# Performance work log

Hardware: AMD Instinct MI355X
Metric: run time of the kernel (lower is better)

The kernel has to match this reference:

```python
import jax, jax.numpy as jnp
import numpy as np


def setup_inputs() -> dict:
    key = jax.random.key(0)
    ks = jax.random.split(key, 6)
    B, T, DIM = 8, 2048, 512
    CB_DIM, CB_SIZE = 256, 8192
    return {
        "x": jax.random.normal(ks[0], (B, T, DIM), dtype=jnp.float32),
        "embed": jax.random.normal(ks[1], (CB_SIZE, CB_DIM), dtype=jnp.float32),
        "W_in": jax.random.normal(ks[2], (CB_DIM, DIM), dtype=jnp.float32) * (1.0 / np.sqrt(DIM)),
        "b_in": jax.random.normal(ks[3], (CB_DIM,), dtype=jnp.float32) * 0.01,
        "W_out": jax.random.normal(ks[4], (DIM, CB_DIM), dtype=jnp.float32) * (1.0 / np.sqrt(CB_DIM)),
        "b_out": jax.random.normal(ks[5], (DIM,), dtype=jnp.float32) * 0.01,
    }


def reference(x, embed, W_in, b_in, W_out, b_out):
    """encode (project_in -> euclidean quantize) then decode (embedding -> project_out).

    Returns (embed_ind [B,T] int32, out [B,T,dim] float).
    """
    B, T, _ = x.shape
    # project_in: Linear(dim -> codebook_dim)
    z = jnp.einsum("btd,cd->btc", x, W_in) + b_in            # [B,T,CB_DIM]
    zf = z.reshape(-1, z.shape[-1])                           # [N,CB_DIM]
    # dist = -(||z||^2 - 2 z.e + ||e||^2); argmax over codebook
    x_sq = jnp.sum(zf * zf, axis=1, keepdims=True)            # [N,1]
    e_sq = jnp.sum(embed * embed, axis=1)                     # [CB_SIZE]
    dist = -(x_sq - 2.0 * (zf @ embed.T) + e_sq[None, :])     # [N,CB_SIZE]
    embed_ind = jnp.argmax(dist, axis=-1).reshape(B, T)       # [B,T]
    # decode: embedding lookup + project_out
    quantize = embed[embed_ind]                               # [B,T,CB_DIM]
    out = jnp.einsum("btc,dc->btd", quantize, W_out) + b_out  # [B,T,dim]
    return embed_ind, out
```

## Files before the change

### kernel.cpp

```cpp
#include <hip/hip_runtime.h>

#define N_TOK 16384
#define DIM   512
#define CBD   256
#define CBS   8192

typedef short short8 __attribute__((ext_vector_type(8)));
typedef float f32x4 __attribute__((ext_vector_type(4)));

#define GLOAD16(g, l) __builtin_amdgcn_global_load_lds( \
    (const __attribute__((address_space(1))) void*)(g), \
    (__attribute__((address_space(3))) void*)(l), 16, 0, 0)

#define VMCNT(n) asm volatile("s_waitcnt vmcnt(" #n ")" ::: "memory")

__device__ inline unsigned short f2bf_rne(float f) {
    unsigned u = __float_as_uint(f);
    unsigned r = (u + 0x7FFFu + ((u >> 16) & 1u)) >> 16;
    return (unsigned short)r;
}
__device__ inline float bf2f(unsigned short h) { return __uint_as_float((unsigned)h << 16); }
__device__ inline short f2h(float f) {
    _Float16 h = (_Float16)f;
    short r; __builtin_memcpy(&r, &h, 2); return r;
}
__device__ inline float h2f(short s) {
    _Float16 h; __builtin_memcpy(&h, &s, 2); return (float)h;
}

template <int LOGK>
__global__ __launch_bounds__(256) void pack_w(const float* __restrict__ src, short* __restrict__ dst) {
    int e = blockIdx.x * 256 + threadIdx.x;
    int r = e >> LOGK, k = e & ((1 << LOGK) - 1);
    float v = src[e];
    unsigned short h = f2bf_rne(v);
    unsigned short l = f2bf_rne(v - bf2f(h));
    size_t base = (size_t)r << (LOGK + 1);
    dst[base + k] = (short)h;
    dst[base + (1 << LOGK) + k] = (short)l;
}

__global__ __launch_bounds__(256) void prep_embed(const float* __restrict__ embed,
                                                  float* __restrict__ esq,
                                                  short* __restrict__ epack,
                                                  short* __restrict__ e16,
                                                  float* __restrict__ denorm) {
    int wave = threadIdx.x >> 6, lane = threadIdx.x & 63;
    int c = (blockIdx.x << 2) + wave;
    float4 v = reinterpret_cast<const float4*>(embed + (size_t)c * CBD)[lane];
    short4 hs, ls, fs;
    {
        unsigned short h, l;
        h = f2bf_rne(v.x); l = f2bf_rne(v.x - bf2f(h)); hs.x = h; ls.x = l;
        h = f2bf_rne(v.y); l = f2bf_rne(v.y - bf2f(h)); hs.y = h; ls.y = l;
        h = f2bf_rne(v.z); l = f2bf_rne(v.z - bf2f(h)); hs.z = h; ls.z = l;
        h = f2bf_rne(v.w); l = f2bf_rne(v.w - bf2f(h)); hs.w = h; ls.w = l;
    }
    fs.x = f2h(v.x); fs.y = f2h(v.y); fs.z = f2h(v.z); fs.w = f2h(v.w);
    reinterpret_cast<short4*>(epack + (size_t)c * 512)[lane] = hs;
    reinterpret_cast<short4*>(epack + (size_t)c * 512 + 256)[lane] = ls;
    reinterpret_cast<short4*>(e16 + (size_t)c * 256)[lane] = fs;
    float s = v.x * v.x + v.y * v.y + v.z * v.z + v.w * v.w;
    float dx = v.x - h2f(fs.x), dy = v.y - h2f(fs.y);
    float dz = v.z - h2f(fs.z), dw = v.w - h2f(fs.w);
    float ds = dx * dx + dy * dy + dz * dz + dw * dw;
    #pragma unroll
    for (int m = 32; m; m >>= 1) { s += __shfl_xor(s, m, 64); ds += __shfl_xor(ds, m, 64); }
    if (!lane) { esq[c] = s; denorm[c] = ds; }
}

__global__ __launch_bounds__(256) void znorm_k(const float* __restrict__ zf32,
                                               const short* __restrict__ z16,
                                               float2* __restrict__ znorm2) {
    int wave = threadIdx.x >> 6, lane = threadIdx.x & 63;
    int r = blockIdx.x * 4 + wave;
    float4 v = reinterpret_cast<const float4*>(zf32 + (size_t)r * 256)[lane];
    short4 h = reinterpret_cast<const short4*>(z16 + (size_t)r * 256)[lane];
    float a = h2f(h.x), b = h2f(h.y), c = h2f(h.z), d = h2f(h.w);
    float s16 = a * a + b * b + c * c + d * d;
    float dx = v.x - a, dy = v.y - b, dz = v.z - c, dw = v.w - d;
    float ds = dx * dx + dy * dy + dz * dz + dw * dw;
    #pragma unroll
    for (int m = 32; m; m >>= 1) { s16 += __shfl_xor(s16, m, 64); ds += __shfl_xor(ds, m, 64); }
    if (!lane) znorm2[r] = make_float2(sqrtf(s16), sqrtf(ds));
}

__global__ __launch_bounds__(256) void maxe_k(const float* __restrict__ esq,
                                              const float* __restrict__ denorm,
                                              float* __restrict__ maxe) {
    float m = 0.f, md = 0.f;
    #pragma unroll
    for (int k = 0; k < 32; ++k) {
        m = fmaxf(m, esq[threadIdx.x + (k << 8)]);
        md = fmaxf(md, denorm[threadIdx.x + (k << 8)]);
    }
    #pragma unroll
    for (int s = 32; s; s >>= 1) {
        m = fmaxf(m, __shfl_xor(m, s, 64));
        md = fmaxf(md, __shfl_xor(md, s, 64));
    }
    __shared__ float w[4], wd[4];
    if (!(threadIdx.x & 63)) { w[threadIdx.x >> 6] = m; wd[threadIdx.x >> 6] = md; }
    __syncthreads();
    if (threadIdx.x == 0) {
        maxe[0] = sqrtf(fmaxf(fmaxf(w[0], w[1]), fmaxf(w[2], w[3])));
        maxe[1] = sqrtf(fmaxf(fmaxf(wd[0], wd[1]), fmaxf(wd[2], wd[3])));
    }
}

__global__ __launch_bounds__(256, 3) void gemm_in_mfma(const short* __restrict__ xpk,
                                                       const short* __restrict__ wpk,
                                                       const float* __restrict__ b_in,
                                                       short* __restrict__ z16,
                                                       float* __restrict__ zf32) {
    __shared__ __align__(16) char smem[49152];
    const int tid = threadIdx.x;
    const int lane = tid & 63, wid = tid >> 6;
    const int l15 = lane & 15, rg = lane >> 4;
    const int bm = blockIdx.x << 6, bn = blockIdx.y << 7;
    const int g = tid & 7, rpb = tid >> 3;

    const char* xb = (const char*)xpk;
    const char* wb = (const char*)wpk;
    const int sw = ((g ^ (rpb & 7)) << 4);
    size_t aoff[2], boff[2][2];
    #pragma unroll
    for (int it = 0; it < 2; ++it)
        aoff[it] = (size_t)(bm + it * 32 + rpb) * 2048 + sw;
    #pragma unroll
    for (int it = 0; it < 4; ++it)
        boff[it >> 1][it & 1] = (size_t)(bn + it * 32 + rpb) * 2048 + sw;

    const int ax0 = ((rg ^ (l15 & 7)) << 4);
    const int ax1 = (((rg + 4) ^ (l15 & 7)) << 4);
    const char* aBase = smem + l15 * 128;
    const char* bBase = smem + 8192 + (wid * 32 + l15) * 128;

    f32x4 acc[4][2] = {};

#define GIN_STAGE(BUF, KT) do { \
    size_t aK = (size_t)(((((KT) >> 4) << 3) | ((KT) & 7))) * 128; \
    size_t bK = (size_t)((((((KT) >> 3) & 1) << 3) | ((KT) & 7))) * 128; \
    char* dA = smem + (BUF) * 24576 + (tid << 4); \
    char* dB = dA + 8192; \
    GLOAD16(xb + aoff[0] + aK, dA); \
    GLOAD16(xb + aoff[1] + aK, dA + 4096); \
    GLOAD16(wb + boff[0][0] + bK, dB); \
    GLOAD16(wb + boff[0][1] + bK, dB + 4096); \
    GLOAD16(wb + boff[1][0] + bK, dB + 8192); \
    GLOAD16(wb + boff[1][1] + bK, dB + 12288); } while (0)

    GIN_STAGE(0, 0);
    VMCNT(0);
    __syncthreads();
    #pragma unroll 1
    for (int kt = 0; kt < 32; ++kt) {
        const int buf = kt & 1;
        if (kt + 1 < 32) GIN_STAGE(buf ^ 1, kt + 1);
        const char* aB = aBase + buf * 24576;
        const char* bB = bBase + buf * 24576;
        #pragma unroll
        for (int ks = 0; ks < 2; ++ks) {
            int ax = ks ? ax1 : ax0;
            short8 aF[4], bF[2];
            #pragma unroll
            for (int mi = 0; mi < 4; ++mi) aF[mi] = *(const short8*)(aB + mi * 2048 + ax);
            #pragma unroll
            for (int ni = 0; ni < 2; ++ni) bF[ni] = *(const short8*)(bB + ni * 2048 + ax);
            #pragma unroll
            for (int mi = 0; mi < 4; ++mi)
                #pragma unroll
                for (int ni = 0; ni < 2; ++ni)
                    acc[mi][ni] = __builtin_amdgcn_mfma_f32_16x16x32_bf16(aF[mi], bF[ni], acc[mi][ni], 0, 0, 0);
        }
        VMCNT(0);
        __syncthreads();
    }
    float bb[2];
    #pragma unroll
    for (int ni = 0; ni < 2; ++ni) bb[ni] = b_in[bn + wid * 32 + ni * 16 + l15];
    #pragma unroll
    for (int mi = 0; mi < 4; ++mi)
        #pragma unroll
        for (int ni = 0; ni < 2; ++ni)
            #pragma unroll
            for (int j = 0; j < 4; ++j) {
                int r = bm + mi * 16 + rg * 4 + j;
                int c = bn + wid * 32 + ni * 16 + l15;
                float s = acc[mi][ni][j] + bb[ni];
                z16[(size_t)r * 256 + c] = f2h(s);
                zf32[(size_t)r * 256 + c] = s;
            }
}

__global__ __launch_bounds__(512, 2) void score_mfma(const short* __restrict__ zpk,
                                                     const short* __restrict__ epk,
                                                     const float* __restrict__ esqg,
                                                     float4* __restrict__ partials) {
    __shared__ __align__(16) char smem[131072];
    const int tid = threadIdx.x;
    const int lane = tid & 63, w = tid >> 6;
    const int l15 = lane & 15, rg = lane >> 4;

    int flat = blockIdx.x;
    int xcd = flat & 7, jb = flat >> 3;
    int g  = xcd >> 1;
    int bX = ((xcd & 1) << 5) + jb;
    const int bm = bX << 8;
    const int C0g = g << 11;

    const char* zb = (const char*)zpk;
    short8 aF0[8], aF1[8];
    #pragma unroll
    for (int ks = 0; ks < 8; ++ks) {
        aF0[ks] = *(const short8*)(zb + (size_t)(bm + w * 32 + l15) * 512 + ks * 64 + rg * 16);
        aF1[ks] = *(const short8*)(zb + (size_t)(bm + w * 32 + 16 + l15) * 512 + ks * 64 + rg * 16);
    }

    const char* eb = (const char*)epk;

#define SCB_STAGE(BUF, T) do { \
    _Pragma("unroll") for (int i_ = 0; i_ < 8; ++i_) { \
        int u_ = i_ * 512 + tid; \
        int col_ = u_ >> 5, slot_ = u_ & 31; \
        const char* s_ = eb + (size_t)(C0g + (T) * 128 + col_) * 512 \
                         + ((slot_ ^ (col_ & 15)) << 4); \
        GLOAD16(s_, smem + (BUF) * 65536 + u_ * 16); \
    } } while (0)

    f32x4 acc0[8] = {};
    f32x4 acc1[8] = {};

    SCB_STAGE(0, 0);
    VMCNT(0);
    __syncthreads();

    #pragma unroll 1
    for (int ch = 0; ch < 16; ++ch) {
        const int buf = ch & 1;
        if (ch < 15) SCB_STAGE(buf ^ 1, ch + 1);
        const char* bB = smem + buf * 65536;
        #pragma unroll
        for (int ks = 0; ks < 8; ++ks) {
            short8 bF[8];
            #pragma unroll
            for (int ni = 0; ni < 8; ++ni)
                bF[ni] = *(const short8*)(bB + (ni * 16 + l15) * 512 +
                                          (((ks * 4 + rg) ^ (l15 & 15)) << 4));
            #pragma unroll
            for (int ni = 0; ni < 8; ++ni) {
                acc0[ni] = __builtin_amdgcn_mfma_f32_16x16x32_f16(aF0[ks], bF[ni], acc0[ni], 0, 0, 0);
                acc1[ni] = __builtin_amdgcn_mfma_f32_16x16x32_f16(aF1[ks], bF[ni], acc1[ni], 0, 0, 0);
            }
        }
        {
            const int cb = C0g + ch * 128 + l15;
            float esq8[8];
            #pragma unroll
            for (int ni = 0; ni < 8; ++ni) esq8[ni] = esqg[cb + ni * 16];
            #pragma unroll
            for (int mi = 0; mi < 2; ++mi)
                #pragma unroll
                for (int j2 = 0; j2 < 4; ++j2) {
                    float v1 = -3.4e38f, v2 = -3.4e38f;
                    int i1 = 0x7fffffff;
                    #pragma unroll
                    for (int ni = 0; ni < 8; ++ni) {
                        float s = fmaf(2.f, mi ? acc1[ni][j2] : acc0[ni][j2], -esq8[ni]);
                        int c = cb + ni * 16;
                        if (s > v1) { v2 = v1; v1 = s; i1 = c; }
                        else if (s > v2) v2 = s;
                    }
                    #pragma unroll
                    for (int m = 1; m < 16; m <<= 1) {
                        float ov1 = __shfl_xor(v1, m, 64);
                        int   oi1 = __shfl_xor(i1, m, 64);
                        float ov2 = __shfl_xor(v2, m, 64);
                        float nv2 = fmaxf(fmaxf(v2, ov2), fminf(v1, ov1));
                        if (ov1 > v1 || (ov1 == v1 && oi1 < i1)) { v1 = ov1; i1 = oi1; }
                        v2 = nv2;
                    }
                    if (l15 == 0) {
                        int row = bm + w * 32 + mi * 16 + rg * 4 + j2;
                        partials[(size_t)(g * 16 + ch) * N_TOK + row] =
                            make_float4(v1, __int_as_float(i1), v2, 0.f);
                    }
                }
            #pragma unroll
            for (int ni = 0; ni < 8; ++ni) {
                acc0[ni] = (f32x4){0.f, 0.f, 0.f, 0.f};
                acc1[ni] = (f32x4){0.f, 0.f, 0.f, 0.f};
            }
        }
        VMCNT(0);
        __syncthreads();
    }
}

__global__ __launch_bounds__(256) void combine(const float4* __restrict__ partials,
                                               const float2* __restrict__ znorm2,
                                               const float* __restrict__ maxe,
                                               int* __restrict__ idx, float* __restrict__ idxf,
                                               float* __restrict__ rescueT) {
    int sub = threadIdx.x & 63;
    int row = blockIdx.x * 4 + (threadIdx.x >> 6);
    float4 p = partials[(size_t)sub * N_TOK + row];
    float v1 = p.x; int i1 = __float_as_int(p.y); float v2 = p.z;
    #pragma unroll
    for (int m = 1; m < 64; m <<= 1) {
        float ov1 = __shfl_xor(v1, m, 64);
        int   oi1 = __shfl_xor(i1, m, 64);
        float ov2 = __shfl_xor(v2, m, 64);
        float nv2 = fmaxf(fmaxf(v2, ov2), fminf(v1, ov1));
        if (ov1 > v1 || (ov1 == v1 && oi1 < i1)) { v1 = ov1; i1 = oi1; }
        v2 = nv2;
    }
    if (sub == 0) {
        float2 zn = znorm2[row];
        float thr = fmaf(2.1f, zn.y * maxe[0] + zn.x * maxe[1], 0.02f);
        idx[row] = i1;
        idxf[row] = (float)i1;
        rescueT[row] = (v1 - v2 <= thr) ? (v1 - thr) : 3.0e38f;
    }
}

__global__ __launch_bounds__(256) void rescue(const float* __restrict__ zf32,
                                              const float* __restrict__ embed,
                                              const float* __restrict__ esq,
                                              const float4* __restrict__ partials,
                                              const float* __restrict__ rescueT,
                                              int* __restrict__ idx, float* __restrict__ idxf) {
    int row = blockIdx.x;
    float t = rescueT[row];
    if (t > 1.0e38f) return;
    __shared__ __align__(16) float zrow[256];
    __shared__ float gv[16];
    __shared__ int   gi[16];
    const int tid = threadIdx.x;
    const int grp = tid >> 4, ln = tid & 15;
    zrow[tid] = zf32[(size_t)row * 256 + tid];
    __syncthreads();
    const float4* zr = (const float4*)zrow;
    float bv = -3.4e38f; int bi = 0x7fffffff;
    for (int nt = 0; nt < 64; ++nt) {
        if (partials[(size_t)nt * N_TOK + row].x < t) continue;
        #pragma unroll 1
        for (int it = 0; it < 8; ++it) {
            int c = nt * 128 + it * 16 + grp;
            const float4* er = (const float4*)(embed + (size_t)c * 256);
            float d = 0.f;
            #pragma unroll
            for (int q = 0; q < 4; ++q) {
                float4 e4 = er[q * 16 + ln];
                float4 z4 = zr[q * 16 + ln];
                d = fmaf(e4.x, z4.x, d); d = fmaf(e4.y, z4.y, d);
                d = fmaf(e4.z, z4.z, d); d = fmaf(e4.w, z4.w, d);
            }
            #pragma unroll
            for (int m = 1; m < 16; m <<= 1) d += __shfl_xor(d, m, 64);
            if (ln == 0) {
                float s = 2.f * d - esq[c];
                if (s > bv || (s == bv && c < bi)) { bv = s; bi = c; }
            }
        }
    }
    if (ln == 0) { gv[grp] = bv; gi[grp] = bi; }
    __syncthreads();
    if (tid == 0) {
        float v = gv[0]; int i = gi[0];
        #pragma unroll
        for (int k = 1; k < 16; ++k)
            if (gv[k] > v || (gv[k] == v && gi[k] < i)) { v = gv[k]; i = gi[k]; }
        idx[row] = i; idxf[row] = (float)i;
    }
}

__global__ __launch_bounds__(256, 2) void gemm_out_mfma(const short* __restrict__ epk,
                                                        const short* __restrict__ wpk,
                                                        const int* __restrict__ idx,
                                                        const float* __restrict__ b_out,
                                                        float* __restrict__ out) {
    __shared__ __align__(16) char smem[65536];
    const int tid = threadIdx.x;
    const int lane = tid & 63, wid = tid >> 6;
    const int wr = wid >> 1, wc = wid & 1;
    const int l15 = lane & 15, rg = lane >> 4;
    const int bm = blockIdx.x << 7, bn = blockIdx.y << 7;
    const int g = tid & 7, rpb = tid >> 3;

    const char* ebp = (const char*)epk;
    const char* wb = (const char*)wpk;
    const int sw = ((g ^ (rpb & 7)) << 4);
    size_t aoff[4], boff[4];
    #pragma unroll
    for (int it = 0; it < 4; ++it) {
        int c = idx[bm + it * 32 + rpb];
        aoff[it] = (size_t)c * 1024 + sw;
        boff[it] = (size_t)(bn + it * 32 + rpb) * 1024 + sw;
    }

    const int ax0 = ((rg ^ (l15 & 7)) << 4);
    const int ax1 = (((rg + 4) ^ (l15 & 7)) << 4);
    const char* aBase = smem + (wr * 64 + l15) * 128;
    const char* bBase = smem + 16384 + (wc * 64 + l15) * 128;

    f32x4 acc[4][4] = {};

#define GOUT_STAGE(BUF, KT) do { \
    size_t aK = (size_t)((((KT) & 3) | (((KT) >> 3) << 2))) * 128; \
    size_t bK = (size_t)((KT) & 7) * 128; \
    char* dA = smem + (BUF) * 32768 + (tid << 4); \
    char* dB = dA + 16384; \
    _Pragma("unroll") for (int it_ = 0; it_ < 4; ++it_) { \
        GLOAD16(ebp + aoff[it_] + aK, dA + it_ * 4096); \
        GLOAD16(wb + boff[it_] + bK, dB + it_ * 4096); } } while (0)

    GOUT_STAGE(0, 0);
    VMCNT(0);
    __syncthreads();
    #pragma unroll 1
    for (int kt = 0; kt < 16; ++kt) {
        const int buf = kt & 1;
        if (kt + 1 < 16) GOUT_STAGE(buf ^ 1, kt + 1);
        const char* aB = aBase + buf * 32768;
        const char* bB = bBase + buf * 32768;
        #pragma unroll
        for (int ks = 0; ks < 2; ++ks) {
            int ax = ks ? ax1 : ax0;
            short8 aF[4], bF[4];
            #pragma unroll
            for (int mi = 0; mi < 4; ++mi) aF[mi] = *(const short8*)(aB + mi * 2048 + ax);
            #pragma unroll
            for (int ni = 0; ni < 4; ++ni) bF[ni] = *(const short8*)(bB + ni * 2048 + ax);
            #pragma unroll
            for (int mi = 0; mi < 4; ++mi)
                #pragma unroll
                for (int ni = 0; ni < 4; ++ni)
                    acc[mi][ni] = __builtin_amdgcn_mfma_f32_16x16x32_bf16(aF[mi], bF[ni], acc[mi][ni], 0, 0, 0);
        }
        VMCNT(0);
        __syncthreads();
    }
    float bb[4];
    #pragma unroll
    for (int ni = 0; ni < 4; ++ni) bb[ni] = b_out[bn + wc * 64 + ni * 16 + l15];
    #pragma unroll
    for (int mi = 0; mi < 4; ++mi)
        #pragma unroll
        for (int ni = 0; ni < 4; ++ni)
            #pragma unroll
            for (int j = 0; j < 4; ++j) {
                int r = bm + wr * 64 + mi * 16 + rg * 4 + j;
                int c = bn + wc * 64 + ni * 16 + l15;
                out[(size_t)r * 512 + c] = acc[mi][ni][j] + bb[ni];
            }
}

__global__ __launch_bounds__(256) void esq_kernel(const float* __restrict__ embed,
                                                  float* __restrict__ esq) {
    int wave = threadIdx.x >> 6, lane = threadIdx.x & 63;
    int c = (blockIdx.x << 2) + wave;
    float4 v = reinterpret_cast<const float4*>(embed + (size_t)c * CBD)[lane];
    float s = v.x * v.x + v.y * v.y + v.z * v.z + v.w * v.w;
    #pragma unroll
    for (int m = 32; m; m >>= 1) s += __shfl_xor(s, m, 64);
    if (!lane) esq[c] = s;
}

template <bool GATHER>
__global__ __launch_bounds__(256) void gemm_nt(const float* __restrict__ A,
                                               const float* __restrict__ B,
                                               const float* __restrict__ bias,
                                               const int* __restrict__ gather,
                                               float* __restrict__ C,
                                               int M, int N, int K) {
    __shared__ __align__(16) float sA[64][68];
    __shared__ __align__(16) float sB[64][68];
    const int tid = threadIdx.x;
    const int tx = tid & 15, ty = tid >> 4;
    const int bm = blockIdx.x << 6, bn = blockIdx.y << 6;
    float acc[4][4] = {};
    for (int k0 = 0; k0 < K; k0 += 64) {
        #pragma unroll
        for (int i = 0; i < 4; ++i) {
            int f = tid + (i << 8);
            int m = f >> 4;
            int k4 = (f & 15) << 2;
            long arow = bm + m;
            if (GATHER) arow = gather[arow];
            float4 v = *reinterpret_cast<const float4*>(A + arow * K + k0 + k4);
            sA[k4 + 0][m] = v.x; sA[k4 + 1][m] = v.y;
            sA[k4 + 2][m] = v.z; sA[k4 + 3][m] = v.w;
            float4 w = *reinterpret_cast<const float4*>(B + (long)(bn + m) * K + k0 + k4);
            sB[k4 + 0][m] = w.x; sB[k4 + 1][m] = w.y;
            sB[k4 + 2][m] = w.z; sB[k4 + 3][m] = w.w;
        }
        __syncthreads();
        #pragma unroll
        for (int kk = 0; kk < 64; ++kk) {
            float4 a = *reinterpret_cast<const float4*>(&sA[kk][ty << 2]);
            float4 b = *reinterpret_cast<const float4*>(&sB[kk][tx << 2]);
            float av[4] = {a.x, a.y, a.z, a.w};
            float bv[4] = {b.x, b.y, b.z, b.w};
            #pragma unroll
            for (int i = 0; i < 4; ++i)
                #pragma unroll
                for (int j = 0; j < 4; ++j)
                    acc[i][j] = fmaf(av[i], bv[j], acc[i][j]);
        }
        __syncthreads();
    }
    #pragma unroll
    for (int i = 0; i < 4; ++i) {
        long m = bm + (ty << 2) + i;
        #pragma unroll
        for (int j = 0; j < 4; ++j) {
            int n = bn + (tx << 2) + j;
            C[m * N + n] = acc[i][j] + bias[n];
        }
    }
}

__global__ __launch_bounds__(256) void score_argmax(const float* __restrict__ z,
                                                    const float* __restrict__ embed,
                                                    const float* __restrict__ esq,
                                                    int* __restrict__ idx_out,
                                                    float* __restrict__ idx_f32) {
    __shared__ __align__(16) float sZ[64][68];
    __shared__ __align__(16) float sE[64][68];
    const int tid = threadIdx.x;
    const int tx = tid & 15, ty = tid >> 4;
    const int bm = blockIdx.x << 6;
    float best[4];
    int bidx[4];
    #pragma unroll
    for (int i = 0; i < 4; ++i) { best[i] = -3.4e38f; bidx[i] = 0; }
    for (int ct = 0; ct < CBS; ct += 64) {
        float acc[4][4] = {};
        for (int k0 = 0; k0 < CBD; k0 += 64) {
            #pragma unroll
            for (int i = 0; i < 4; ++i) {
                int f = tid + (i << 8);
                int m = f >> 4;
                int k4 = (f & 15) << 2;
                float4 v = *reinterpret_cast<const float4*>(z + (long)(bm + m) * CBD + k0 + k4);
                sZ[k4 + 0][m] = v.x; sZ[k4 + 1][m] = v.y;
                sZ[k4 + 2][m] = v.z; sZ[k4 + 3][m] = v.w;
                float4 w = *reinterpret_cast<const float4*>(embed + (long)(ct + m) * CBD + k0 + k4);
                sE[k4 + 0][m] = w.x; sE[k4 + 1][m] = w.y;
                sE[k4 + 2][m] = w.z; sE[k4 + 3][m] = w.w;
            }
            __syncthreads();
            #pragma unroll
            for (int kk = 0; kk < 64; ++kk) {
                float4 a = *reinterpret_cast<const float4*>(&sZ[kk][ty << 2]);
                float4 b = *reinterpret_cast<const float4*>(&sE[kk][tx << 2]);
                float av[4] = {a.x, a.y, a.z, a.w};
                float bv[4] = {b.x, b.y, b.z, b.w};
                #pragma unroll
                for (int i = 0; i < 4; ++i)
                    #pragma unroll
                    for (int j = 0; j < 4; ++j)
                        acc[i][j] = fmaf(av[i], bv[j], acc[i][j]);
            }
            __syncthreads();
        }
        #pragma unroll
        for (int j = 0; j < 4; ++j) {
            int c = ct + (tx << 2) + j;
            float eq = esq[c];
            #pragma unroll
            for (int i = 0; i < 4; ++i) {
                float s = 2.0f * acc[i][j] - eq;
                if (s > best[i] || (s == best[i] && c < bidx[i])) { best[i] = s; bidx[i] = c; }
            }
        }
    }
    #pragma unroll
    for (int i = 0; i < 4; ++i) {
        float b = best[i];
        int bi = bidx[i];
        #pragma unroll
        for (int m = 1; m < 16; m <<= 1) {
            float ob = __shfl_xor(b, m, 64);
            int oi = __shfl_xor(bi, m, 64);
            if (ob > b || (ob == b && oi < bi)) { b = ob; bi = oi; }
        }
        if (tx == 0) {
            int row = bm + (ty << 2) + i;
            idx_out[row] = bi;
            idx_f32[row] = (float)bi;
        }
    }
}

extern "C" void kernel_launch(void* const* d_in, const int* in_sizes, int n_in,
                              void* d_out, int out_size, void* d_ws, size_t ws_size,
                              hipStream_t stream) {
    const float* x     = (const float*)d_in[0];
    const float* embed = (const float*)d_in[1];
    const float* W_in  = (const float*)d_in[2];
    const float* b_in  = (const float*)d_in[3];
    const float* W_out = (const float*)d_in[4];
    const float* b_out = (const float*)d_in[5];

    float* out_idx = (float*)d_out;
    float* out     = (float*)d_out + N_TOK;

    char* ws = (char*)d_ws;
    float*  esq      = (float*)ws;
    float*  rescueT  = (float*)(ws + 32768);
    int*    idx      = (int*)(ws + 98304);
    float2* znorm2   = (float2*)(ws + 163840);
    float*  denorm   = (float*)(ws + 294912);
    float*  maxe     = (float*)(ws + 327680);
    short*  xpack    = (short*)(ws + 327936);
    float4* partials = (float4*)(ws + 327936);
    float*  zf32     = (float*)(ws + 327936 + 33554432);
    short*  z16      = (short*)((char*)zf32 + 16777216);
    short*  e16      = z16 + (size_t)N_TOK * 256;
    short*  epack    = e16 + (size_t)CBS * 256;
    short*  winpk    = epack + (size_t)CBS * 512;
    short*  wopk     = winpk + (size_t)CBD * 1024;
    size_t need = (size_t)((char*)(wopk + (size_t)DIM * 512) - ws);

    if (ws_size >= need) {
        pack_w<9><<<(N_TOK * DIM) / 256, 256, 0, stream>>>(x, xpack);
        pack_w<9><<<(CBD * DIM) / 256, 256, 0, stream>>>(W_in, winpk);
        pack_w<8><<<(DIM * CBD) / 256, 256, 0, stream>>>(W_out, wopk);
        prep_embed<<<CBS / 4, 256, 0, stream>>>(embed, esq, epack, e16, denorm);
        maxe_k<<<1, 256, 0, stream>>>(esq, denorm, maxe);
        gemm_in_mfma<<<dim3(N_TOK / 64, 2), 256, 0, stream>>>(xpack, winpk, b_in, z16, zf32);
        znorm_k<<<N_TOK / 4, 256, 0, stream>>>(zf32, z16, znorm2);
        score_mfma<<<256, 512, 0, stream>>>(z16, e16, esq, partials);
        combine<<<N_TOK / 4, 256, 0, stream>>>(partials, znorm2, maxe, idx, out_idx, rescueT);
        rescue<<<N_TOK, 256, 0, stream>>>(zf32, embed, esq, partials, rescueT, idx, out_idx);
        gemm_out_mfma<<<dim3(N_TOK / 128, 4), 256, 0, stream>>>(epack, wopk, idx, b_out, out);
    } else {
        float* z   = (float*)d_ws;
        float* es  = z + (size_t)N_TOK * CBD;
        int*   id  = (int*)(es + CBS);
        gemm_nt<false><<<dim3(N_TOK / 64, CBD / 64), 256, 0, stream>>>(
            x, W_in, b_in, nullptr, z, N_TOK, CBD, DIM);
        esq_kernel<<<CBS / 4, 256, 0, stream>>>(embed, es);
        score_argmax<<<N_TOK / 64, 256, 0, stream>>>(z, embed, es, id, out_idx);
        gemm_nt<true><<<dim3(N_TOK / 64, DIM / 64), 256, 0, stream>>>(
            embed, W_out, b_out, id, out, N_TOK, DIM, CBD);
    }
}
```

Baseline: 278.4 us.

## Halve score block to 256 threads with K-split half-chunk LDS double buffering

The score kernel now uses 256-thread blocks covering 128 token rows, launched as 512 blocks instead of 256. Each 128-code chunk of the codebook is split into two K halves held in 32 KB LDS buffers, for 64 KB per block instead of 128 KB. Loads for the next half overlap the MFMAs on the current half. This aims to fit more blocks per CU and raise occupancy, at the cost of more frequent barriers and each codebook tile being reused across fewer rows.

```diff
diff --git a/kernel.cpp b/kernel.cpp
--- a/kernel.cpp
+++ b/kernel.cpp
@@ -193,11 +193,11 @@
             }
 }
 
-__global__ __launch_bounds__(512, 2) void score_mfma(const short* __restrict__ zpk,
+__global__ __launch_bounds__(256, 2) void score_mfma(const short* __restrict__ zpk,
                                                      const short* __restrict__ epk,
                                                      const float* __restrict__ esqg,
                                                      float4* __restrict__ partials) {
-    __shared__ __align__(16) char smem[131072];
+    __shared__ __align__(16) char smem[65536];
     const int tid = threadIdx.x;
     const int lane = tid & 63, w = tid >> 6;
     const int l15 = lane & 15, rg = lane >> 4;
@@ -205,8 +205,8 @@
     int flat = blockIdx.x;
     int xcd = flat & 7, jb = flat >> 3;
     int g  = xcd >> 1;
-    int bX = ((xcd & 1) << 5) + jb;
-    const int bm = bX << 8;
+    int bX = ((xcd & 1) << 6) + jb;
+    const int bm = bX << 7;
     const int C0g = g << 11;
 
     const char* zb = (const char*)zpk;
@@ -219,42 +219,45 @@
 
     const char* eb = (const char*)epk;
 
-#define SCB_STAGE(BUF, T) do { \
+#define SCB_STAGE(BUF, T, H) do { \
     _Pragma("unroll") for (int i_ = 0; i_ < 8; ++i_) { \
-        int u_ = i_ * 512 + tid; \
-        int col_ = u_ >> 5, slot_ = u_ & 31; \
-        const char* s_ = eb + (size_t)(C0g + (T) * 128 + col_) * 512 \
+        int u_ = i_ * 256 + tid; \
+        int col_ = u_ >> 4, slot_ = u_ & 15; \
+        const char* s_ = eb + (size_t)(C0g + (T) * 128 + col_) * 512 + (H) * 256 \
                          + ((slot_ ^ (col_ & 15)) << 4); \
-        GLOAD16(s_, smem + (BUF) * 65536 + u_ * 16); \
+        GLOAD16(s_, smem + (BUF) * 32768 + u_ * 16); \
+    } } while (0)
+
+#define SC_PHASE(BUF, KS0) do { \
+    const char* bB = smem + (BUF) * 32768; \
+    _Pragma("unroll") for (int ksl = 0; ksl < 4; ++ksl) { \
+        short8 bF[8]; \
+        _Pragma("unroll") for (int ni = 0; ni < 8; ++ni) \
+            bF[ni] = *(const short8*)(bB + (ni * 16 + l15) * 256 + \
+                                      (((ksl * 4 + rg) ^ (l15 & 15)) << 4)); \
+        _Pragma("unroll") for (int ni = 0; ni < 8; ++ni) { \
+            acc0[ni] = __builtin_amdgcn_mfma_f32_16x16x32_f16(aF0[(KS0) + ksl], bF[ni], acc0[ni], 0, 0, 0); \
+            acc1[ni] = __builtin_amdgcn_mfma_f32_16x16x32_f16(aF1[(KS0) + ksl], bF[ni], acc1[ni], 0, 0, 0); \
+        } \
     } } while (0)
 
     f32x4 acc0[8] = {};
     f32x4 acc1[8] = {};
 
-    SCB_STAGE(0, 0);
+    SCB_STAGE(0, 0, 0);
     VMCNT(0);
     __syncthreads();
 
     #pragma unroll 1
-    for (int ch = 0; ch < 16; ++ch) {
-        const int buf = ch & 1;
-        if (ch < 15) SCB_STAGE(buf ^ 1, ch + 1);
-        const char* bB = smem + buf * 65536;
-        #pragma unroll
-        for (int ks = 0; ks < 8; ++ks) {
-            short8 bF[8];
-            #pragma unroll
-            for (int ni = 0; ni < 8; ++ni)
-                bF[ni] = *(const short8*)(bB + (ni * 16 + l15) * 512 +
-                                          (((ks * 4 + rg) ^ (l15 & 15)) << 4));
-            #pragma unroll
-            for (int ni = 0; ni < 8; ++ni) {
-                acc0[ni] = __builtin_amdgcn_mfma_f32_16x16x32_f16(aF0[ks], bF[ni], acc0[ni], 0, 0, 0);
-                acc1[ni] = __builtin_amdgcn_mfma_f32_16x16x32_f16(aF1[ks], bF[ni], acc1[ni], 0, 0, 0);
-            }
-        }
+    for (int t = 0; t < 16; ++t) {
+        SCB_STAGE(1, t, 1);
+        SC_PHASE(0, 0);
+        VMCNT(0);
+        __syncthreads();
+        if (t < 15) SCB_STAGE(0, t + 1, 0);
+        SC_PHASE(1, 4);
         {
-            const int cb = C0g + ch * 128 + l15;
+            const int cb = C0g + t * 128 + l15;
             float esq8[8];
             #pragma unroll
             for (int ni = 0; ni < 8; ++ni) esq8[ni] = esqg[cb + ni * 16];
@@ -282,7 +285,7 @@
                     }
                     if (l15 == 0) {
                         int row = bm + w * 32 + mi * 16 + rg * 4 + j2;
-                        partials[(size_t)(g * 16 + ch) * N_TOK + row] =
+                        partials[(size_t)(g * 16 + t) * N_TOK + row] =
                             make_float4(v1, __int_as_float(i1), v2, 0.f);
                     }
                 }
@@ -632,7 +635,7 @@
         maxe_k<<<1, 256, 0, stream>>>(esq, denorm, maxe);
         gemm_in_mfma<<<dim3(N_TOK / 64, 2), 256, 0, stream>>>(xpack, winpk, b_in, z16, zf32);
         znorm_k<<<N_TOK / 4, 256, 0, stream>>>(zf32, z16, znorm2);
-        score_mfma<<<256, 512, 0, stream>>>(z16, e16, esq, partials);
+        score_mfma<<<512, 256, 0, stream>>>(z16, e16, esq, partials);
         combine<<<N_TOK / 4, 256, 0, stream>>>(partials, znorm2, maxe, idx, out_idx, rescueT);
         rescue<<<N_TOK, 256, 0, stream>>>(zf32, embed, esq, partials, rescueT, idx, out_idx);
         gemm_out_mfma<<<dim3(N_TOK / 128, 4), 256, 0, stream>>>(epack, wopk, idx, b_out, out);
```

Result: no change. 279.8 us (+0.5%).
